# Kernel tuning notes

Measured on AMD Instinct MI355X. Metric: run time of the kernel, lower is better.

## Reference

```python
import jax, jax.numpy as jnp
import numpy as np

B, T_ENC, D = 64, 1000, 512
V, L, H, E = 5000, 150, 512, 512
PAD = 0


def setup_inputs() -> dict:
    key = jax.random.key(0)
    ks = jax.random.split(key, 12)
    s = 1.0 / np.sqrt(H)
    inp = {
        "enc_output": jax.random.normal(ks[0], (B, T_ENC, D), jnp.float32),
        "enc_len": jax.random.randint(ks[1], (B,), T_ENC // 2, T_ENC + 1, jnp.int32),
        "dec_in": jax.random.randint(ks[2], (B, L), 0, V, jnp.int32),
        "dec_out": jax.random.randint(ks[3], (B, L), 0, V, jnp.int32),
        # learned parameters (PyTorch LSTMCell layout: gates i,f,g,o stacked)
        "emb_table": jax.random.normal(ks[4], (V, E), jnp.float32).at[PAD].set(0.0),
        "W_ih": jax.random.uniform(ks[5], (4 * H, E + D), jnp.float32, -s, s),
        "b_ih": jax.random.uniform(ks[6], (4 * H,), jnp.float32, -s, s),
        "W_hh": jax.random.uniform(ks[7], (4 * H, H), jnp.float32, -s, s),
        "b_hh": jax.random.uniform(ks[8], (4 * H,), jnp.float32, -s, s),
        "W_out": jax.random.uniform(ks[9], (V, H), jnp.float32, -s, s),
        "b_out": jax.random.uniform(ks[10], (V,), jnp.float32, -s, s),
    }
    return inp


def reference(enc_output, enc_len, dec_in, dec_out, emb_table,
              W_ih, b_ih, W_hh, b_hh, W_out, b_out):
    # teacher forcing (tf_rate=1.0), eval mode (dropout = identity)
    dt = enc_output.dtype
    # embedding with padding_idx=PAD -> zero vector for pad tokens
    emb_seq = emb_table[dec_in] * (dec_in != PAD)[..., None].astype(dt)  # [B,L,E]
    valid = (jnp.arange(T_ENC)[None, :] < enc_len[:, None])  # [B,T]

    def step(carry, emb_t):
        h, c = carry
        # masked dot-product attention over encoder states
        scores = jnp.einsum('btd,bd->bt', enc_output, h)
        scores = jnp.where(valid, scores, jnp.asarray(-1e9, dt))
        attn = jax.nn.softmax(scores, axis=-1)                # [B,T]
        ctx = jnp.einsum('bt,btd->bd', attn, enc_output)      # [B,D]
        x = jnp.concatenate([emb_t, ctx], axis=-1)            # [B,E+D]
        gates = x @ W_ih.T + b_ih + h @ W_hh.T + b_hh         # [B,4H]
        i, f, g, o = jnp.split(gates, 4, axis=-1)
        c2 = jax.nn.sigmoid(f) * c + jax.nn.sigmoid(i) * jnp.tanh(g)
        h2 = jax.nn.sigmoid(o) * jnp.tanh(c2)
        logit = h2 @ W_out.T + b_out                          # [B,V]
        return (h2, c2), (logit, attn)

    init = (jnp.zeros((B, H), dt), jnp.zeros((B, H), dt))
    _, (logits, attns) = jax.lax.scan(step, init, jnp.swapaxes(emb_seq, 0, 1))
    logits = jnp.swapaxes(logits, 0, 1)                       # [B,L,V]
    attns = jnp.swapaxes(attns, 0, 1)                         # [B,L,T]
    log_probs = jax.nn.log_softmax(logits, axis=2)
    dec_lp = jnp.take_along_axis(log_probs, dec_out[..., None].astype(jnp.int32), axis=2)[..., 0]
    prediction = jnp.argmax(logits, axis=-1)
    return logits, dec_lp, prediction, attns
```

## Files before the change

### kernel.cpp

```cpp
#include <hip/hip_runtime.h>
#include <math.h>

#define B_ 64
#define T_ 1000
#define D_ 512
#define V_ 5000
#define L_ 150
#define H_ 512

#define OFF_SCORES 0u
#define OFF_PM     64000u
#define OFF_PL     65280u
#define OFF_PCTX   66560u
#define OFF_XT     721920u
#define OFF_H      787456u
#define OFF_HT     820224u
#define OFF_C      852992u
#define OFF_GP     885760u
#define OFF_LP     1672192u
#define OFF_ST     2312192u

#define OUT_LOGITS 0ull
#define OUT_DECLP  48000000ull
#define OUT_PRED   48009600ull
#define OUT_ATTN   48019200ull

__global__ __launch_bounds__(256) void k_attn(const float* __restrict__ enc,
                                              const int* __restrict__ enc_len,
                                              float* __restrict__ ws) {
  const int c = blockIdx.x;
  const int b = blockIdx.y;
  const int lane = threadIdx.x & 63;
  const int w = threadIdx.x >> 6;
  const int tid = threadIdx.x;

  const float* __restrict__ hb = ws + OFF_H + b * 512;
  const float4 h0 = *(const float4*)(hb + lane * 4);
  const float4 h1 = *(const float4*)(hb + 256 + lane * 4);

  float4 a0 = make_float4(0.f, 0.f, 0.f, 0.f);
  float4 a1 = make_float4(0.f, 0.f, 0.f, 0.f);
  float m = -3e38f, l = 0.f;
  const int len = enc_len[b];
  const int t0 = c * 50;
  float* __restrict__ scores = ws + OFF_SCORES + b * 1000;

  for (int t = t0 + w; t < t0 + 50; t += 4) {
    const bool valid = (t < len);
    float s;
    float4 e0, e1;
    if (valid) {
      const float* __restrict__ ep = enc + ((size_t)b * 1000 + t) * 512;
      e0 = *(const float4*)(ep + lane * 4);
      e1 = *(const float4*)(ep + 256 + lane * 4);
      float p = e0.x * h0.x + e0.y * h0.y + e0.z * h0.z + e0.w * h0.w
              + e1.x * h1.x + e1.y * h1.y + e1.z * h1.z + e1.w * h1.w;
      #pragma unroll
      for (int off = 1; off < 64; off <<= 1) p += __shfl_xor(p, off);
      s = p;
    } else {
      s = -1e9f;
      e0 = make_float4(0.f, 0.f, 0.f, 0.f);
      e1 = make_float4(0.f, 0.f, 0.f, 0.f);
    }
    if (lane == 0) scores[t] = s;
    if (valid) {
      const float mn = fmaxf(m, s);
      const float sc = expf(m - mn);
      const float wt = expf(s - mn);
      l = l * sc + wt;
      m = mn;
      a0.x = a0.x * sc + wt * e0.x; a0.y = a0.y * sc + wt * e0.y;
      a0.z = a0.z * sc + wt * e0.z; a0.w = a0.w * sc + wt * e0.w;
      a1.x = a1.x * sc + wt * e1.x; a1.y = a1.y * sc + wt * e1.y;
      a1.z = a1.z * sc + wt * e1.z; a1.w = a1.w * sc + wt * e1.w;
    }
  }

  __shared__ float sctx[4 * 512];
  __shared__ float sm[4], sl[4];
  sctx[w * 512 + lane * 4 + 0] = a0.x;
  sctx[w * 512 + lane * 4 + 1] = a0.y;
  sctx[w * 512 + lane * 4 + 2] = a0.z;
  sctx[w * 512 + lane * 4 + 3] = a0.w;
  sctx[w * 512 + 256 + lane * 4 + 0] = a1.x;
  sctx[w * 512 + 256 + lane * 4 + 1] = a1.y;
  sctx[w * 512 + 256 + lane * 4 + 2] = a1.z;
  sctx[w * 512 + 256 + lane * 4 + 3] = a1.w;
  if (lane == 0) { sm[w] = m; sl[w] = l; }
  __syncthreads();

  const float M = fmaxf(fmaxf(sm[0], sm[1]), fmaxf(sm[2], sm[3]));
  const float f0 = expf(sm[0] - M), f1 = expf(sm[1] - M);
  const float f2 = expf(sm[2] - M), f3 = expf(sm[3] - M);
  float* __restrict__ pctx = ws + OFF_PCTX + ((size_t)c * 64 + b) * 512;
  for (int d = tid; d < 512; d += 256) {
    pctx[d] = sctx[d] * f0 + sctx[512 + d] * f1 + sctx[1024 + d] * f2 + sctx[1536 + d] * f3;
  }
  if (tid == 0) {
    ws[OFF_PM + c * 64 + b] = M;
    ws[OFF_PL + c * 64 + b] = sl[0] * f0 + sl[1] * f1 + sl[2] * f2 + sl[3] * f3;
  }
}

__global__ __launch_bounds__(256) void k_comb(const float* __restrict__ emb_table,
                                              const int* __restrict__ dec_in,
                                              const int* __restrict__ dec_out,
                                              float* __restrict__ ws,
                                              float* __restrict__ out, int t) {
  const int b = blockIdx.x;
  const int tid = threadIdx.x;
  __shared__ float fm[79], fl[79], fv[79];
  __shared__ int   fi[79];
  __shared__ float ef[20], spm[20], spl[20];
  __shared__ float sMS[2];

  if (t > 0) {
    const int tp = t - 1;
    if (tid < 79) {
      const float4 st = *(const float4*)(ws + OFF_ST + ((size_t)tid * 64 + b) * 4);
      fm[tid] = st.x; fl[tid] = st.y; fv[tid] = st.z; fi[tid] = (int)st.w;
    }
    __syncthreads();
    if (tid == 0) {
      float M = -3e38f;
      for (int c2 = 0; c2 < 79; ++c2) M = fmaxf(M, fm[c2]);
      float S = 0.f, bv = -3e38f;
      int bi = 0;
      for (int c2 = 0; c2 < 79; ++c2) {
        S += fl[c2] * expf(fm[c2] - M);
        if (fv[c2] > bv) { bv = fv[c2]; bi = fi[c2]; }
      }
      const float lse = logf(S) + M;
      const int tok = dec_out[b * 150 + tp];
      const float lg = out[OUT_LOGITS + ((size_t)b * 150 + tp) * 5000 + tok];
      out[OUT_DECLP + (size_t)b * 150 + tp] = lg - lse;
      out[OUT_PRED  + (size_t)b * 150 + tp] = (float)bi;
    }
    __syncthreads();
  }
  if (t >= 150) return;

  if (tid < 20) {
    spm[tid] = ws[OFF_PM + tid * 64 + b];
    spl[tid] = ws[OFF_PL + tid * 64 + b];
  }
  __syncthreads();
  if (tid == 0) {
    float M = -3e38f;
    for (int c = 0; c < 20; ++c) M = fmaxf(M, spm[c]);
    float S = 0.f;
    for (int c = 0; c < 20; ++c) {
      const float e = expf(spm[c] - M);
      ef[c] = e;
      S += spl[c] * e;
    }
    sMS[0] = M; sMS[1] = S;
  }
  __syncthreads();
  const float M = sMS[0];
  const float invS = 1.f / sMS[1];

  for (int d = tid; d < 512; d += 256) {
    float acc = 0.f;
    #pragma unroll
    for (int c = 0; c < 20; ++c)
      acc += ws[OFF_PCTX + ((size_t)c * 64 + b) * 512 + d] * ef[c];
    ws[OFF_XT + (size_t)(512 + d) * 64 + b] = acc * invS;
  }
  const int tok = dec_in[b * 150 + t];
  const float* __restrict__ er = emb_table + (size_t)tok * 512;
  for (int k = tid; k < 512; k += 256)
    ws[OFF_XT + (size_t)k * 64 + b] = (tok != 0) ? er[k] : 0.f;
  float* __restrict__ ao = out + OUT_ATTN + ((size_t)b * 150 + t) * 1000;
  const float* __restrict__ sc = ws + OFF_SCORES + b * 1000;
  for (int tt = tid; tt < 1000; tt += 256)
    ao[tt] = expf(sc[tt] - M) * invS;
}

__global__ __launch_bounds__(256) void k_gates(const float* __restrict__ W_ih,
                                               const float* __restrict__ W_hh,
                                               float* __restrict__ ws) {
  const int w = blockIdx.x * 4 + (threadIdx.x >> 6);
  const int lane = threadIdx.x & 63;
  const int rg = w & 255;
  const int kc = w >> 8;
  const int r0 = rg * 8;

  const float* __restrict__ Wp;
  const float* __restrict__ xp;
  int ld, kofs;
  if (kc < 4) { Wp = W_ih; ld = 1024; kofs = kc * 256; xp = ws + OFF_XT + (size_t)kofs * 64; }
  else        { Wp = W_hh; ld = 512;  kofs = (kc - 4) * 256; xp = ws + OFF_HT + (size_t)kofs * 64; }

  float acc[8] = {0.f, 0.f, 0.f, 0.f, 0.f, 0.f, 0.f, 0.f};
  for (int k = 0; k < 256; k += 4) {
    const float x0 = xp[(k + 0) * 64 + lane];
    const float x1 = xp[(k + 1) * 64 + lane];
    const float x2 = xp[(k + 2) * 64 + lane];
    const float x3 = xp[(k + 3) * 64 + lane];
    #pragma unroll
    for (int r = 0; r < 8; ++r) {
      const float4 wv = *(const float4*)(Wp + (size_t)(r0 + r) * ld + kofs + k);
      acc[r] += wv.x * x0 + wv.y * x1 + wv.z * x2 + wv.w * x3;
    }
  }
  float* __restrict__ gp = ws + OFF_GP + ((size_t)kc * 2048 + r0) * 64;
  #pragma unroll
  for (int r = 0; r < 8; ++r) gp[r * 64 + lane] = acc[r];
}

__global__ __launch_bounds__(256) void k_cell(const float* __restrict__ b_ih,
                                              const float* __restrict__ b_hh,
                                              float* __restrict__ ws) {
  const int g = blockIdx.x * 256 + threadIdx.x;
  const int b = g & 63;
  const int hi = g >> 6;
  float ai = b_ih[hi]        + b_hh[hi];
  float af = b_ih[hi + 512]  + b_hh[hi + 512];
  float ag = b_ih[hi + 1024] + b_hh[hi + 1024];
  float ao = b_ih[hi + 1536] + b_hh[hi + 1536];
  #pragma unroll
  for (int kc = 0; kc < 6; ++kc) {
    const float* __restrict__ gp = ws + OFF_GP + (size_t)kc * 2048 * 64;
    ai += gp[(hi       ) * 64 + b];
    af += gp[(hi +  512) * 64 + b];
    ag += gp[(hi + 1024) * 64 + b];
    ao += gp[(hi + 1536) * 64 + b];
  }
  const float cp = ws[OFF_C + b * 512 + hi];
  const float ig = 1.f / (1.f + expf(-ai));
  const float fg = 1.f / (1.f + expf(-af));
  const float gg = tanhf(ag);
  const float og = 1.f / (1.f + expf(-ao));
  const float c2 = fg * cp + ig * gg;
  const float h2 = og * tanhf(c2);
  ws[OFF_C + b * 512 + hi] = c2;
  ws[OFF_H + b * 512 + hi] = h2;
  ws[OFF_HT + (size_t)hi * 64 + b] = h2;
}

__global__ __launch_bounds__(256) void k_logits(const float* __restrict__ W_out,
                                                float* __restrict__ ws) {
  const int w = blockIdx.x * 4 + (threadIdx.x >> 6);
  if (w >= 1250) return;
  const int lane = threadIdx.x & 63;
  const int vg = w % 625;
  const int ks = w / 625;
  const int v0 = vg * 8;
  const int k0 = ks * 256;
  const float* __restrict__ hT = ws + OFF_HT;
  float acc[8] = {0.f, 0.f, 0.f, 0.f, 0.f, 0.f, 0.f, 0.f};
  for (int k = k0; k < k0 + 256; k += 4) {
    const float x0 = hT[(k + 0) * 64 + lane];
    const float x1 = hT[(k + 1) * 64 + lane];
    const float x2 = hT[(k + 2) * 64 + lane];
    const float x3 = hT[(k + 3) * 64 + lane];
    #pragma unroll
    for (int r = 0; r < 8; ++r) {
      const float4 wv = *(const float4*)(W_out + (size_t)(v0 + r) * 512 + k);
      acc[r] += wv.x * x0 + wv.y * x1 + wv.z * x2 + wv.w * x3;
    }
  }
  float* __restrict__ lp = ws + OFF_LP + ((size_t)ks * 5000 + v0) * 64;
  #pragma unroll
  for (int r = 0; r < 8; ++r) lp[r * 64 + lane] = acc[r];
}

__global__ __launch_bounds__(256) void k_lcomb(const float* __restrict__ b_out,
                                               float* __restrict__ ws,
                                               float* __restrict__ out, int t) {
  const int vc = blockIdx.x;
  const int v0 = vc * 64;
  const int NV = (5000 - v0 < 64) ? (5000 - v0) : 64;
  const int tid = threadIdx.x;
  __shared__ float Ls[64 * 65];

  #pragma unroll
  for (int e = 0; e < 16; ++e) {
    const int idx = e * 256 + tid;
    const int v = idx >> 6, b = idx & 63;
    if (v < NV) {
      Ls[v * 65 + b] = ws[OFF_LP + (size_t)(v0 + v) * 64 + b]
                     + ws[OFF_LP + (size_t)(5000 + v0 + v) * 64 + b]
                     + b_out[v0 + v];
    }
  }
  __syncthreads();
  #pragma unroll
  for (int e = 0; e < 16; ++e) {
    const int idx = e * 256 + tid;
    const int v = idx & 63, b = idx >> 6;
    if (v < NV)
      out[OUT_LOGITS + ((size_t)b * 150 + t) * 5000 + v0 + v] = Ls[v * 65 + b];
  }
  if (tid < 64) {
    const int b = tid;
    float m = -3e38f, l = 0.f, bv = -3e38f;
    int bi = 0;
    for (int v = 0; v < NV; ++v) {
      const float val = Ls[v * 65 + b];
      const float mn = fmaxf(m, val);
      l = l * expf(m - mn) + expf(val - mn);
      m = mn;
      if (val > bv) { bv = val; bi = v0 + v; }
    }
    const float4 st = make_float4(m, l, bv, (float)bi);
    *(float4*)(ws + OFF_ST + ((size_t)vc * 64 + b) * 4) = st;
  }
}

extern "C" void kernel_launch(void* const* d_in, const int* in_sizes, int n_in,
                              void* d_out, int out_size, void* d_ws, size_t ws_size,
                              hipStream_t stream) {
  const float* enc     = (const float*)d_in[0];
  const int*   enc_len = (const int*)d_in[1];
  const int*   dec_in  = (const int*)d_in[2];
  const int*   dec_out = (const int*)d_in[3];
  const float* emb     = (const float*)d_in[4];
  const float* W_ih    = (const float*)d_in[5];
  const float* b_ih    = (const float*)d_in[6];
  const float* W_hh    = (const float*)d_in[7];
  const float* b_hh    = (const float*)d_in[8];
  const float* W_out   = (const float*)d_in[9];
  const float* b_out   = (const float*)d_in[10];
  float* out = (float*)d_out;
  float* ws  = (float*)d_ws;

  hipMemsetAsync(ws + OFF_H, 0, (size_t)(3 * 32768) * sizeof(float), stream);

  for (int t = 0; t < 150; ++t) {
    k_attn  <<<dim3(20, 64), 256, 0, stream>>>(enc, enc_len, ws);
    k_comb  <<<64,  256, 0, stream>>>(emb, dec_in, dec_out, ws, out, t);
    k_gates <<<384, 256, 0, stream>>>(W_ih, W_hh, ws);
    k_cell  <<<128, 256, 0, stream>>>(b_ih, b_hh, ws);
    k_logits<<<313, 256, 0, stream>>>(W_out, ws);
    k_lcomb <<<79,  256, 0, stream>>>(b_out, ws, out, t);
  }
  k_comb<<<64, 256, 0, stream>>>(emb, dec_in, dec_out, ws, out, 150);
}
```

Before: 19.42 ms.

## Fuse decoder steps into one persistent cooperative kernel with grid barriers

Replaces the six launches per timestep with a single cooperative persistent kernel. It uses software grid barriers and overlaps independent stages: next-step attention runs alongside the logits GEMV, and the logits combine/final reduction run alongside the comb and gates stages. The per-chunk online log-sum-exp state is replaced by a block-wide argmax/LSE pass over the stored logits row, and explicit fmaf calls are used throughout. This is meant to remove kernel launch overhead and idle gaps between small stages. In exchange it adds spin-barrier cost and caps the grid at 512 blocks, which may limit parallelism in the attention phase.

```diff
diff --git a/kernel.cpp b/kernel.cpp
--- a/kernel.cpp
+++ b/kernel.cpp
@@ -1,12 +1,6 @@
 #include <hip/hip_runtime.h>
 #include <math.h>
 
-#define B_ 64
-#define T_ 1000
-#define D_ 512
-#define V_ 5000
-#define L_ 150
-#define H_ 512
 
 #define OFF_SCORES 0u
 #define OFF_PM     64000u
@@ -18,21 +12,43 @@
 #define OFF_C      852992u
 #define OFF_GP     885760u
 #define OFF_LP     1672192u
-#define OFF_ST     2312192u
+#define WS_BAR     2332416u
 
 #define OUT_LOGITS 0ull
 #define OUT_DECLP  48000000ull
 #define OUT_PRED   48009600ull
 #define OUT_ATTN   48019200ull
 
-__global__ __launch_bounds__(256) void k_attn(const float* __restrict__ enc,
-                                              const int* __restrict__ enc_len,
-                                              float* __restrict__ ws) {
-  const int c = blockIdx.x;
-  const int b = blockIdx.y;
+__device__ __forceinline__ void gbar(int* __restrict__ bar, int nblk) {
+  __syncthreads();
+  if (threadIdx.x == 0) {
+    __threadfence();
+    int g = __hip_atomic_load(&bar[1], __ATOMIC_RELAXED, __HIP_MEMORY_SCOPE_AGENT);
+    int prev = __hip_atomic_fetch_add(&bar[0], 1, __ATOMIC_ACQ_REL, __HIP_MEMORY_SCOPE_AGENT);
+    if (prev == nblk - 1) {
+      __hip_atomic_store(&bar[0], 0, __ATOMIC_RELAXED, __HIP_MEMORY_SCOPE_AGENT);
+      __hip_atomic_store(&bar[1], g + 1, __ATOMIC_RELEASE, __HIP_MEMORY_SCOPE_AGENT);
+    } else {
+      while (__hip_atomic_load(&bar[1], __ATOMIC_ACQUIRE, __HIP_MEMORY_SCOPE_AGENT) == g) {
+        __builtin_amdgcn_s_sleep(2);
+      }
+    }
+    __threadfence();
+  }
+  __syncthreads();
+}
+
+__device__ void d_attn(int job, const float* __restrict__ enc,
+                       const int* __restrict__ enc_len,
+                       float* __restrict__ ws, float* __restrict__ smem) {
+  const int c = job >> 6;
+  const int b = job & 63;
   const int lane = threadIdx.x & 63;
   const int w = threadIdx.x >> 6;
   const int tid = threadIdx.x;
+  float* sctx = smem;
+  float* sm   = smem + 2048;
+  float* sl   = smem + 2052;
 
   const float* __restrict__ hb = ws + OFF_H + b * 512;
   const float4 h0 = *(const float4*)(hb + lane * 4);
@@ -53,8 +69,14 @@
       const float* __restrict__ ep = enc + ((size_t)b * 1000 + t) * 512;
       e0 = *(const float4*)(ep + lane * 4);
       e1 = *(const float4*)(ep + 256 + lane * 4);
-      float p = e0.x * h0.x + e0.y * h0.y + e0.z * h0.z + e0.w * h0.w
-              + e1.x * h1.x + e1.y * h1.y + e1.z * h1.z + e1.w * h1.w;
+      float p = e0.x * h0.x;
+      p = fmaf(e0.y, h0.y, p);
+      p = fmaf(e0.z, h0.z, p);
+      p = fmaf(e0.w, h0.w, p);
+      p = fmaf(e1.x, h1.x, p);
+      p = fmaf(e1.y, h1.y, p);
+      p = fmaf(e1.z, h1.z, p);
+      p = fmaf(e1.w, h1.w, p);
       #pragma unroll
       for (int off = 1; off < 64; off <<= 1) p += __shfl_xor(p, off);
       s = p;
@@ -68,17 +90,15 @@
       const float mn = fmaxf(m, s);
       const float sc = expf(m - mn);
       const float wt = expf(s - mn);
-      l = l * sc + wt;
+      l = fmaf(l, sc, wt);
       m = mn;
-      a0.x = a0.x * sc + wt * e0.x; a0.y = a0.y * sc + wt * e0.y;
-      a0.z = a0.z * sc + wt * e0.z; a0.w = a0.w * sc + wt * e0.w;
-      a1.x = a1.x * sc + wt * e1.x; a1.y = a1.y * sc + wt * e1.y;
-      a1.z = a1.z * sc + wt * e1.z; a1.w = a1.w * sc + wt * e1.w;
-    }
-  }
-
-  __shared__ float sctx[4 * 512];
-  __shared__ float sm[4], sl[4];
+      a0.x = fmaf(a0.x, sc, wt * e0.x); a0.y = fmaf(a0.y, sc, wt * e0.y);
+      a0.z = fmaf(a0.z, sc, wt * e0.z); a0.w = fmaf(a0.w, sc, wt * e0.w);
+      a1.x = fmaf(a1.x, sc, wt * e1.x); a1.y = fmaf(a1.y, sc, wt * e1.y);
+      a1.z = fmaf(a1.z, sc, wt * e1.z); a1.w = fmaf(a1.w, sc, wt * e1.w);
+    }
+  }
+
   sctx[w * 512 + lane * 4 + 0] = a0.x;
   sctx[w * 512 + lane * 4 + 1] = a0.y;
   sctx[w * 512 + lane * 4 + 2] = a0.z;
@@ -95,51 +115,27 @@
   const float f2 = expf(sm[2] - M), f3 = expf(sm[3] - M);
   float* __restrict__ pctx = ws + OFF_PCTX + ((size_t)c * 64 + b) * 512;
   for (int d = tid; d < 512; d += 256) {
-    pctx[d] = sctx[d] * f0 + sctx[512 + d] * f1 + sctx[1024 + d] * f2 + sctx[1536 + d] * f3;
+    float v = sctx[d] * f0;
+    v = fmaf(sctx[512 + d], f1, v);
+    v = fmaf(sctx[1024 + d], f2, v);
+    v = fmaf(sctx[1536 + d], f3, v);
+    pctx[d] = v;
   }
   if (tid == 0) {
     ws[OFF_PM + c * 64 + b] = M;
-    ws[OFF_PL + c * 64 + b] = sl[0] * f0 + sl[1] * f1 + sl[2] * f2 + sl[3] * f3;
-  }
-}
-
-__global__ __launch_bounds__(256) void k_comb(const float* __restrict__ emb_table,
-                                              const int* __restrict__ dec_in,
-                                              const int* __restrict__ dec_out,
-                                              float* __restrict__ ws,
-                                              float* __restrict__ out, int t) {
-  const int b = blockIdx.x;
+    ws[OFF_PL + c * 64 + b] = fmaf(sl[3], f3, fmaf(sl[2], f2, fmaf(sl[1], f1, sl[0] * f0)));
+  }
+}
+
+__device__ void d_comb(int b, int t, const float* __restrict__ emb_table,
+                       const int* __restrict__ dec_in,
+                       float* __restrict__ ws, float* __restrict__ out,
+                       float* __restrict__ smem) {
   const int tid = threadIdx.x;
-  __shared__ float fm[79], fl[79], fv[79];
-  __shared__ int   fi[79];
-  __shared__ float ef[20], spm[20], spl[20];
-  __shared__ float sMS[2];
-
-  if (t > 0) {
-    const int tp = t - 1;
-    if (tid < 79) {
-      const float4 st = *(const float4*)(ws + OFF_ST + ((size_t)tid * 64 + b) * 4);
-      fm[tid] = st.x; fl[tid] = st.y; fv[tid] = st.z; fi[tid] = (int)st.w;
-    }
-    __syncthreads();
-    if (tid == 0) {
-      float M = -3e38f;
-      for (int c2 = 0; c2 < 79; ++c2) M = fmaxf(M, fm[c2]);
-      float S = 0.f, bv = -3e38f;
-      int bi = 0;
-      for (int c2 = 0; c2 < 79; ++c2) {
-        S += fl[c2] * expf(fm[c2] - M);
-        if (fv[c2] > bv) { bv = fv[c2]; bi = fi[c2]; }
-      }
-      const float lse = logf(S) + M;
-      const int tok = dec_out[b * 150 + tp];
-      const float lg = out[OUT_LOGITS + ((size_t)b * 150 + tp) * 5000 + tok];
-      out[OUT_DECLP + (size_t)b * 150 + tp] = lg - lse;
-      out[OUT_PRED  + (size_t)b * 150 + tp] = (float)bi;
-    }
-    __syncthreads();
-  }
-  if (t >= 150) return;
+  float* ef  = smem;
+  float* spm = smem + 32;
+  float* spl = smem + 64;
+  float* sMS = smem + 96;
 
   if (tid < 20) {
     spm[tid] = ws[OFF_PM + tid * 64 + b];
@@ -153,7 +149,7 @@
     for (int c = 0; c < 20; ++c) {
       const float e = expf(spm[c] - M);
       ef[c] = e;
-      S += spl[c] * e;
+      S = fmaf(spl[c], e, S);
     }
     sMS[0] = M; sMS[1] = S;
   }
@@ -165,7 +161,7 @@
     float acc = 0.f;
     #pragma unroll
     for (int c = 0; c < 20; ++c)
-      acc += ws[OFF_PCTX + ((size_t)c * 64 + b) * 512 + d] * ef[c];
+      acc = fmaf(ws[OFF_PCTX + ((size_t)c * 64 + b) * 512 + d], ef[c], acc);
     ws[OFF_XT + (size_t)(512 + d) * 64 + b] = acc * invS;
   }
   const int tok = dec_in[b * 150 + t];
@@ -178,10 +174,81 @@
     ao[tt] = expf(sc[tt] - M) * invS;
 }
 
-__global__ __launch_bounds__(256) void k_gates(const float* __restrict__ W_ih,
-                                               const float* __restrict__ W_hh,
-                                               float* __restrict__ ws) {
-  const int w = blockIdx.x * 4 + (threadIdx.x >> 6);
+__device__ void d_lcomb(int vc, int t, const float* __restrict__ b_out,
+                        float* __restrict__ ws, float* __restrict__ out,
+                        float* __restrict__ smem) {
+  const int v0 = vc * 64;
+  const int NV = (5000 - v0 < 64) ? (5000 - v0) : 64;
+  const int tid = threadIdx.x;
+  float* Ls = smem;
+
+  #pragma unroll
+  for (int e = 0; e < 16; ++e) {
+    const int idx = e * 256 + tid;
+    const int v = idx >> 6, b = idx & 63;
+    if (v < NV) {
+      Ls[v * 65 + b] = ws[OFF_LP + (size_t)(v0 + v) * 64 + b]
+                     + ws[OFF_LP + (size_t)(5000 + v0 + v) * 64 + b]
+                     + b_out[v0 + v];
+    }
+  }
+  __syncthreads();
+  #pragma unroll
+  for (int e = 0; e < 16; ++e) {
+    const int idx = e * 256 + tid;
+    const int v = idx & 63, b = idx >> 6;
+    if (v < NV)
+      out[OUT_LOGITS + ((size_t)b * 150 + t) * 5000 + v0 + v] = Ls[v * 65 + b];
+  }
+}
+
+__device__ void d_lfinal(int b, int tp, const int* __restrict__ dec_out,
+                         float* __restrict__ out, float* __restrict__ smem) {
+  const int tid = threadIdx.x;
+  float* sv = smem;
+  float* si = smem + 256;
+  const float* __restrict__ lrow = out + OUT_LOGITS + ((size_t)b * 150 + tp) * 5000;
+
+  float m = -3e38f;
+  int bi = 0;
+  for (int v = tid; v < 5000; v += 256) {
+    const float val = lrow[v];
+    if (val > m) { m = val; bi = v; }
+  }
+  sv[tid] = m;
+  si[tid] = (float)bi;
+  __syncthreads();
+  for (int s = 128; s > 0; s >>= 1) {
+    if (tid < s) {
+      const float vo = sv[tid + s], io = si[tid + s];
+      if (vo > sv[tid] || (vo == sv[tid] && io < si[tid])) { sv[tid] = vo; si[tid] = io; }
+    }
+    __syncthreads();
+  }
+  const float M = sv[0];
+  const int amax = (int)si[0];
+  __syncthreads();
+
+  float s = 0.f;
+  for (int v = tid; v < 5000; v += 256) s += expf(lrow[v] - M);
+  sv[tid] = s;
+  __syncthreads();
+  for (int st = 128; st > 0; st >>= 1) {
+    if (tid < st) sv[tid] += sv[tid + st];
+    __syncthreads();
+  }
+  if (tid == 0) {
+    const float lse = logf(sv[0]) + M;
+    const int tok = dec_out[b * 150 + tp];
+    out[OUT_DECLP + (size_t)b * 150 + tp] = lrow[tok] - lse;
+    out[OUT_PRED  + (size_t)b * 150 + tp] = (float)amax;
+  }
+  __syncthreads();
+}
+
+__device__ void d_gates(int job, const float* __restrict__ W_ih,
+                        const float* __restrict__ W_hh, float* __restrict__ ws) {
+  const int w = job * 4 + (threadIdx.x >> 6);
   const int lane = threadIdx.x & 63;
   const int rg = w & 255;
   const int kc = w >> 8;
@@ -202,7 +269,12 @@
     #pragma unroll
     for (int r = 0; r < 8; ++r) {
       const float4 wv = *(const float4*)(Wp + (size_t)(r0 + r) * ld + kofs + k);
-      acc[r] += wv.x * x0 + wv.y * x1 + wv.z * x2 + wv.w * x3;
+      float a = acc[r];
+      a = fmaf(wv.x, x0, a);
+      a = fmaf(wv.y, x1, a);
+      a = fmaf(wv.z, x2, a);
+      a = fmaf(wv.w, x3, a);
+      acc[r] = a;
     }
   }
   float* __restrict__ gp = ws + OFF_GP + ((size_t)kc * 2048 + r0) * 64;
@@ -210,10 +282,9 @@
   for (int r = 0; r < 8; ++r) gp[r * 64 + lane] = acc[r];
 }
 
-__global__ __launch_bounds__(256) void k_cell(const float* __restrict__ b_ih,
-                                              const float* __restrict__ b_hh,
-                                              float* __restrict__ ws) {
-  const int g = blockIdx.x * 256 + threadIdx.x;
+__device__ void d_cell(int job, const float* __restrict__ b_ih,
+                       const float* __restrict__ b_hh, float* __restrict__ ws) {
+  const int g = job * 256 + threadIdx.x;
   const int b = g & 63;
   const int hi = g >> 6;
   float ai = b_ih[hi]        + b_hh[hi];
@@ -233,16 +304,16 @@
   const float fg = 1.f / (1.f + expf(-af));
   const float gg = tanhf(ag);
   const float og = 1.f / (1.f + expf(-ao));
-  const float c2 = fg * cp + ig * gg;
+  const float c2 = fmaf(fg, cp, ig * gg);
   const float h2 = og * tanhf(c2);
   ws[OFF_C + b * 512 + hi] = c2;
   ws[OFF_H + b * 512 + hi] = h2;
   ws[OFF_HT + (size_t)hi * 64 + b] = h2;
 }
 
-__global__ __launch_bounds__(256) void k_logits(const float* __restrict__ W_out,
-                                                float* __restrict__ ws) {
-  const int w = blockIdx.x * 4 + (threadIdx.x >> 6);
+__device__ void d_logits(int job, const float* __restrict__ W_out,
+                         float* __restrict__ ws) {
+  const int w = job * 4 + (threadIdx.x >> 6);
   if (w >= 1250) return;
   const int lane = threadIdx.x & 63;
   const int vg = w % 625;
@@ -259,7 +330,12 @@
     #pragma unroll
     for (int r = 0; r < 8; ++r) {
       const float4 wv = *(const float4*)(W_out + (size_t)(v0 + r) * 512 + k);
-      acc[r] += wv.x * x0 + wv.y * x1 + wv.z * x2 + wv.w * x3;
+      float a = acc[r];
+      a = fmaf(wv.x, x0, a);
+      a = fmaf(wv.y, x1, a);
+      a = fmaf(wv.z, x2, a);
+      a = fmaf(wv.w, x3, a);
+      acc[r] = a;
     }
   }
   float* __restrict__ lp = ws + OFF_LP + ((size_t)ks * 5000 + v0) * 64;
@@ -267,47 +343,102 @@
   for (int r = 0; r < 8; ++r) lp[r * 64 + lane] = acc[r];
 }
 
-__global__ __launch_bounds__(256) void k_lcomb(const float* __restrict__ b_out,
-                                               float* __restrict__ ws,
-                                               float* __restrict__ out, int t) {
-  const int vc = blockIdx.x;
-  const int v0 = vc * 64;
-  const int NV = (5000 - v0 < 64) ? (5000 - v0) : 64;
-  const int tid = threadIdx.x;
-  __shared__ float Ls[64 * 65];
-
-  #pragma unroll
-  for (int e = 0; e < 16; ++e) {
-    const int idx = e * 256 + tid;
-    const int v = idx >> 6, b = idx & 63;
-    if (v < NV) {
-      Ls[v * 65 + b] = ws[OFF_LP + (size_t)(v0 + v) * 64 + b]
-                     + ws[OFF_LP + (size_t)(5000 + v0 + v) * 64 + b]
-                     + b_out[v0 + v];
-    }
-  }
-  __syncthreads();
-  #pragma unroll
-  for (int e = 0; e < 16; ++e) {
-    const int idx = e * 256 + tid;
-    const int v = idx & 63, b = idx >> 6;
-    if (v < NV)
-      out[OUT_LOGITS + ((size_t)b * 150 + t) * 5000 + v0 + v] = Ls[v * 65 + b];
-  }
-  if (tid < 64) {
-    const int b = tid;
-    float m = -3e38f, l = 0.f, bv = -3e38f;
-    int bi = 0;
-    for (int v = 0; v < NV; ++v) {
-      const float val = Ls[v * 65 + b];
-      const float mn = fmaxf(m, val);
-      l = l * expf(m - mn) + expf(val - mn);
-      m = mn;
-      if (val > bv) { bv = val; bi = v0 + v; }
-    }
-    const float4 st = make_float4(m, l, bv, (float)bi);
-    *(float4*)(ws + OFF_ST + ((size_t)vc * 64 + b) * 4) = st;
-  }
+__global__ __launch_bounds__(256, 2) void k_persist(
+    const float* __restrict__ enc, const int* __restrict__ enc_len,
+    const int* __restrict__ dec_in, const int* __restrict__ dec_out,
+    const float* __restrict__ emb, const float* __restrict__ W_ih,
+    const float* __restrict__ b_ih, const float* __restrict__ W_hh,
+    const float* __restrict__ b_hh, const float* __restrict__ W_out,
+    const float* __restrict__ b_out, float* __restrict__ ws,
+    float* __restrict__ out) {
+  __shared__ float smem[64 * 65];
+  const int bid = blockIdx.x;
+  const int nb = gridDim.x;
+  int* bar = (int*)(ws + WS_BAR);
+
+  for (int job = bid; job < 1280; job += nb) {
+    __syncthreads();
+    d_attn(job, enc, enc_len, ws, smem);
+  }
+  gbar(bar, nb);
+
+  for (int t = 0; t < 150; ++t) {
+    {
+      const int nj = (t > 0) ? 143 : 64;
+      for (int job = bid; job < nj; job += nb) {
+        __syncthreads();
+        if (job < 64) d_comb(job, t, emb, dec_in, ws, out, smem);
+        else          d_lcomb(job - 64, t - 1, b_out, ws, out, smem);
+      }
+    }
+    gbar(bar, nb);
+    {
+      const int nj = (t > 0) ? 448 : 384;
+      for (int job = bid; job < nj; job += nb) {
+        __syncthreads();
+        if (job < 384) d_gates(job, W_ih, W_hh, ws);
+        else           d_lfinal(job - 384, t - 1, dec_out, out, smem);
+      }
+    }
+    gbar(bar, nb);
+    for (int job = bid; job < 128; job += nb) d_cell(job, b_ih, b_hh, ws);
+    gbar(bar, nb);
+    {
+      const int na = (t < 149) ? 1280 : 0;
+      const int nj = na + 313;
+      for (int job = bid; job < nj; job += nb) {
+        __syncthreads();
+        if (job < na) d_attn(job, enc, enc_len, ws, smem);
+        else          d_logits(job - na, W_out, ws);
+      }
+    }
+    gbar(bar, nb);
+  }
+  for (int job = bid; job < 79; job += nb) {
+    __syncthreads();
+    d_lcomb(job, 149, b_out, ws, out, smem);
+  }
+  gbar(bar, nb);
+  for (int job = bid; job < 64; job += nb) {
+    __syncthreads();
+    d_lfinal(job, 149, dec_out, out, smem);
+  }
+}
+
+__global__ __launch_bounds__(256) void k_attn_g(const float* __restrict__ enc,
+                                                const int* __restrict__ enc_len,
+                                                float* __restrict__ ws) {
+  __shared__ float smem[2056];
+  d_attn(blockIdx.x * 64 + blockIdx.y, enc, enc_len, ws, smem);
+}
+__global__ __launch_bounds__(256) void k_comb_g(const float* __restrict__ emb,
+                                                const int* __restrict__ dec_in,
+                                                const int* __restrict__ dec_out,
+                                                float* __restrict__ ws,
+                                                float* __restrict__ out, int t) {
+  __shared__ float smem[512];
+  if (t > 0) { d_lfinal(blockIdx.x, t - 1, dec_out, out, smem); __syncthreads(); }
+  if (t < 150) d_comb(blockIdx.x, t, emb, dec_in, ws, out, smem);
+}
+__global__ __launch_bounds__(256) void k_gates_g(const float* __restrict__ W_ih,
+                                                 const float* __restrict__ W_hh,
+                                                 float* __restrict__ ws) {
+  d_gates(blockIdx.x, W_ih, W_hh, ws);
+}
+__global__ __launch_bounds__(256) void k_cell_g(const float* __restrict__ b_ih,
+                                                const float* __restrict__ b_hh,
+                                                float* __restrict__ ws) {
+  d_cell(blockIdx.x, b_ih, b_hh, ws);
+}
+__global__ __launch_bounds__(256) void k_logits_g(const float* __restrict__ W_out,
+                                                  float* __restrict__ ws) {
+  d_logits(blockIdx.x, W_out, ws);
+}
+__global__ __launch_bounds__(256) void k_lcomb_g(const float* __restrict__ b_out,
+                                                 float* __restrict__ ws,
+                                                 float* __restrict__ out, int t) {
+  __shared__ float smem[64 * 65];
+  d_lcomb(blockIdx.x, t, b_out, ws, out, smem);
 }
 
 extern "C" void kernel_launch(void* const* d_in, const int* in_sizes, int n_in,
@@ -328,14 +459,40 @@
   float* ws  = (float*)d_ws;
 
   hipMemsetAsync(ws + OFF_H, 0, (size_t)(3 * 32768) * sizeof(float), stream);
-
-  for (int t = 0; t < 150; ++t) {
-    k_attn  <<<dim3(20, 64), 256, 0, stream>>>(enc, enc_len, ws);
-    k_comb  <<<64,  256, 0, stream>>>(emb, dec_in, dec_out, ws, out, t);
-    k_gates <<<384, 256, 0, stream>>>(W_ih, W_hh, ws);
-    k_cell  <<<128, 256, 0, stream>>>(b_ih, b_hh, ws);
-    k_logits<<<313, 256, 0, stream>>>(W_out, ws);
-    k_lcomb <<<79,  256, 0, stream>>>(b_out, ws, out, t);
-  }
-  k_comb<<<64, 256, 0, stream>>>(emb, dec_in, dec_out, ws, out, 150);
-}
+  hipMemsetAsync(ws + WS_BAR, 0, 2 * sizeof(int), stream);
+
+  int dev = 0;
+  (void)hipGetDevice(&dev);
+  int numCU = 0, maxb = 0;
+  (void)hipDeviceGetAttribute(&numCU, hipDeviceAttributeMultiprocessorCount, dev);
+  hipError_t eo = hipOccupancyMaxActiveBlocksPerMultiprocessor(
+      &maxb, (const void*)k_persist, 256, 0);
+  if (eo != hipSuccess) maxb = 0;
+  long nbl = (long)maxb * (long)(numCU > 0 ? numCU : 0);
+  int nb = (nbl > 512) ? 512 : (int)nbl;
+
+  bool done = false;
+  if (nb >= 8) {
+    void* args[] = {
+      (void*)&enc, (void*)&enc_len, (void*)&dec_in, (void*)&dec_out, (void*)&emb,
+      (void*)&W_ih, (void*)&b_ih, (void*)&W_hh, (void*)&b_hh, (void*)&W_out,
+      (void*)&b_out, (void*)&ws, (void*)&out
+    };
+    hipError_t el = hipLaunchCooperativeKernel((const void*)k_persist, dim3(nb),
+                                               dim3(256), args, 0, stream);
+    if (el == hipSuccess) done = true;
+    else (void)hipGetLastError();
+  }
+
+  if (!done) {
+    for (int t = 0; t < 150; ++t) {
+      k_attn_g  <<<dim3(20, 64), 256, 0, stream>>>(enc, enc_len, ws);
+      k_comb_g  <<<64,  256, 0, stream>>>(emb, dec_in, dec_out, ws, out, t);
+      k_gates_g <<<384, 256, 0, stream>>>(W_ih, W_hh, ws);
+      k_cell_g  <<<128, 256, 0, stream>>>(b_ih, b_hh, ws);
+      k_logits_g<<<313, 256, 0, stream>>>(W_out, ws);
+      k_lcomb_g <<<79,  256, 0, stream>>>(b_out, ws, out, t);
+    }
+    k_comb_g<<<64, 256, 0, stream>>>(emb, dec_in, dec_out, ws, out, 150);
+  }
+}
```

Measured after the change: 73.55 ms. +278.8%, slower.
